# Kernel tuning notes

Measured on AMD Instinct MI355X. Metric: run time of the kernel, lower is better.

Reference implementation:

```python
import jax, jax.numpy as jnp
import numpy as np

H = 1024   # hidden_size == embedding_dim (forced by the 2*hidden concat/view)
A = 256    # attention_hidden_size
V = 50257  # vocab_size
L = 2      # num_layers
T = 512    # decoder length
S = 512    # encoder length


def setup_inputs() -> dict:
    key = jax.random.key(0)
    ks = jax.random.split(key, 24)
    f = lambda i, shape: (0.02 * jax.random.normal(ks[i], shape)).astype(jnp.float32)
    return {
        "decoder_input": jax.random.randint(ks[0], (T,), 0, V),
        "encoder_outputs": jax.random.normal(ks[1], (S, H), dtype=jnp.float32),
        "emb": f(2, (V, H)),
        # attn (context attention over encoder outputs): Linear(2H->A) split into x/ctx parts, v: Linear(A->1)
        "Wa_x": f(3, (A, H)), "Wa_c": f(4, (A, H)), "ba": f(5, (A,)), "va": f(6, (A,)), "vab": f(7, ()),
        # GRU cells (torch GRUCell param layout: [r; z; n] stacked, 3H rows)
        "Wih0": f(8, (3 * H, 2 * H)), "bih0": f(9, (3 * H,)), "Whh0": f(10, (3 * H, H)), "bhh0": f(11, (3 * H,)),
        "Wih1": f(12, (3 * H, H)), "bih1": f(13, (3 * H,)), "Whh1": f(14, (3 * H, H)), "bhh1": f(15, (3 * H,)),
        # per-layer hidden self-attentions (no context)
        "Wh": f(16, (L, A, H)), "bh": f(17, (L, A)), "vh": f(18, (L, A)), "vhb": f(19, (L,)),
        # output head
        "Wf1": f(20, (32, H)), "bf1": f(21, (32,)), "Wf2": f(22, (V, 32)), "bf2": f(23, (V,)),
    }


def _attn(x, Wx, b, v, vb, ctx=None, Wc=None):
    # additive attention: e_t = v . tanh(W_x x_t + W_c c + b); weighted sum over axis 0
    pre = x @ Wx.T + b                      # [T, A]
    if ctx is not None:
        pre = pre + ctx @ Wc.T              # broadcast [A]
    e = jnp.tanh(pre) @ v + vb              # [T]
    return jax.nn.softmax(e) @ x            # [D]


def _gru(x, h, Wih, bih, Whh, bhh):
    gi = Wih @ x + bih
    gh = Whh @ h + bhh
    ir, iz, inn = jnp.split(gi, 3)
    hr, hz, hn = jnp.split(gh, 3)
    r = jax.nn.sigmoid(ir + hr)
    z = jax.nn.sigmoid(iz + hz)
    n = jnp.tanh(inn + r * hn)
    return (1.0 - z) * n + z * h


def reference(decoder_input, encoder_outputs, emb, Wa_x, Wa_c, ba, va, vab,
              Wih0, bih0, Whh0, bhh0, Wih1, bih1, Whh1, bhh1,
              Wh, bh, vh, vhb, Wf1, bf1, Wf2, bf2):
    tok_embs = emb[decoder_input]           # [T, H]

    def step(carry, tok):
        h0, h1 = carry
        a = _attn(encoder_outputs, Wa_x, ba, va, vab, ctx=h0, Wc=Wa_c)  # [H]
        x = jnp.concatenate([a, tok])                                   # [2H]
        nh0 = _gru(x, h0, Wih0, bih0, Whh0, bhh0)
        nh1 = _gru(nh0, h1, Wih1, bih1, Whh1, bhh1)
        # hidden attention i combines new_h_s[i:]
        h0n = _attn(jnp.stack([nh0, nh1]), Wh[0], bh[0], vh[0], vhb[0])
        h1n = _attn(nh1[None, :], Wh[1], bh[1], vh[1], vhb[1])           # softmax over 1 elem == nh1
        fc1 = jax.nn.relu(Wf1 @ h1n + bf1)                               # dropout = eval-mode identity
        out = jax.nn.softmax(Wf2 @ fc1 + bf2)                            # softmax over vocab (dim 0)
        return (h0n, h1n), out

    h0 = jnp.zeros((Whh0.shape[1],), jnp.float32)
    _, outs = jax.lax.scan(step, (h0, h0), tok_embs)
    return outs  # [T, V]
```

## Files before the change

kernel.cpp:

```cpp
#include <hip/hip_runtime.h>
#include <cstdint>
#include <cstddef>

#define T_LEN 512
#define S_LEN 512
#define HID   1024
#define AD    256
#define VOC   50257
#define G3    3072
#define NWG   256
#define NT    512
#define NPART (197*4)

typedef unsigned long long u64;

#define WS_GENC   0
#define WS_GITOK  (WS_GENC + G3*S_LEN)
#define WS_EX     (WS_GITOK + T_LEN*G3)
#define WS_H1     (WS_EX + S_LEN*AD)
#define WS_FC1    (WS_H1 + T_LEN*HID)
#define WS_ROWP   (WS_FC1 + T_LEN*32)
#define WS_INV    (WS_ROWP + T_LEN*NPART)
#define WS_TAGF   (((WS_INV + T_LEN) + 3) & ~3)

#define SP 2
#define TG_NH0 0
#define TG_NH1 (TG_NH0 + 2*1024*SP)
#define TG_W   (TG_NH1 + 2*1024*SP)
#define TG_U0  (TG_W   + 2*512*SP)
#define TG_U1  (TG_U0  + 2*256*SP)
#define TG_E0  (TG_U1  + 2*256*SP)
#define TG_E1  (TG_E0  + 2*256*SP)
#define TG_TOT (TG_E1  + 2*256*SP)

__device__ inline float wred64(float v) {
  v += __shfl_xor(v, 32, 64); v += __shfl_xor(v, 16, 64); v += __shfl_xor(v, 8, 64);
  v += __shfl_xor(v, 4, 64);  v += __shfl_xor(v, 2, 64);  v += __shfl_xor(v, 1, 64);
  return v;
}
__device__ inline float fast_sigmoid(float x) { return 1.f / (1.f + __expf(-x)); }
__device__ inline float fast_tanh(float x) {
  float e = __expf(2.f * x);
  return 1.f - 2.f / (e + 1.f);
}

__device__ inline u64 ald(const u64* p) {
  return __hip_atomic_load(p, __ATOMIC_RELAXED, __HIP_MEMORY_SCOPE_AGENT);
}
__device__ inline void stq(u64* p, float v, unsigned tag) {
  __hip_atomic_store(p, ((u64)tag << 32) | (u64)__float_as_uint(v),
                     __ATOMIC_RELAXED, __HIP_MEMORY_SCOPE_AGENT);
}
__device__ inline float poll1(const u64* p, unsigned tag) {
  u64 x = ald(p);
  while ((unsigned)(x >> 32) != tag) { __builtin_amdgcn_s_sleep(1); x = ald(p); }
  return __uint_as_float((unsigned)x);
}
__device__ inline void poll2(const u64* p0, const u64* p1, unsigned tag, float& r0, float& r1) {
  u64 x0 = ald(p0), x1 = ald(p1);
  while (((unsigned)(x0 >> 32) != tag) | ((unsigned)(x1 >> 32) != tag)) {
    __builtin_amdgcn_s_sleep(1); x0 = ald(p0); x1 = ald(p1);
  }
  r0 = __uint_as_float((unsigned)x0); r1 = __uint_as_float((unsigned)x1);
}
__device__ inline void poll4(const u64* p0, const u64* p1, const u64* p2, const u64* p3,
                             unsigned tag, float& r0, float& r1, float& r2, float& r3) {
  u64 x0 = ald(p0), x1 = ald(p1), x2 = ald(p2), x3 = ald(p3);
  while (((unsigned)(x0 >> 32) != tag) | ((unsigned)(x1 >> 32) != tag) |
         ((unsigned)(x2 >> 32) != tag) | ((unsigned)(x3 >> 32) != tag)) {
    __builtin_amdgcn_s_sleep(1);
    x0 = ald(p0); x1 = ald(p1); x2 = ald(p2); x3 = ald(p3);
  }
  r0 = __uint_as_float((unsigned)x0); r1 = __uint_as_float((unsigned)x1);
  r2 = __uint_as_float((unsigned)x2); r3 = __uint_as_float((unsigned)x3);
}

__device__ inline float qdot4(const float4& a0, const float4& a1, const float4& a2, const float4& a3,
                              const float4& x0, const float4& x1, const float4& x2, const float4& x3) {
  float a = 0.f;
  a = fmaf(a0.x, x0.x, a); a = fmaf(a0.y, x0.y, a); a = fmaf(a0.z, x0.z, a); a = fmaf(a0.w, x0.w, a);
  a = fmaf(a1.x, x1.x, a); a = fmaf(a1.y, x1.y, a); a = fmaf(a1.z, x1.z, a); a = fmaf(a1.w, x1.w, a);
  a = fmaf(a2.x, x2.x, a); a = fmaf(a2.y, x2.y, a); a = fmaf(a2.z, x2.z, a); a = fmaf(a2.w, x2.w, a);
  a = fmaf(a3.x, x3.x, a); a = fmaf(a3.y, x3.y, a); a = fmaf(a3.z, x3.z, a); a = fmaf(a3.w, x3.w, a);
  return a;
}
__device__ inline float qdot2(const float4& a0, const float4& a1,
                              const float4& x0, const float4& x1) {
  float a = 0.f;
  a = fmaf(a0.x, x0.x, a); a = fmaf(a0.y, x0.y, a); a = fmaf(a0.z, x0.z, a); a = fmaf(a0.w, x0.w, a);
  a = fmaf(a1.x, x1.x, a); a = fmaf(a1.y, x1.y, a); a = fmaf(a1.z, x1.z, a); a = fmaf(a1.w, x1.w, a);
  return a;
}

__global__ void k_init(float* ws) {
  u64* TG = (u64*)(ws + WS_TAGF);
  const int i = blockIdx.x * 256 + threadIdx.x;
  if (i < TG_TOT) TG[i] = 0ull;
}

__global__ __launch_bounds__(256) void k_gemm(
    const float* __restrict__ A, int lda, const int* __restrict__ gidx,
    const float* __restrict__ B, int ldb, int kofs,
    const float* __restrict__ bias, float* __restrict__ C, int ldc,
    int M, int N, int act)
{
  __shared__ float As[64][33];
  __shared__ float Bs[64][33];
  const int bm = blockIdx.y * 64, bn = blockIdx.x * 64;
// ... 34 lines not shown
      acc[2][0]=fmaf(a2,b0,acc[2][0]); acc[2][1]=fmaf(a2,b1,acc[2][1]); acc[2][2]=fmaf(a2,b2,acc[2][2]); acc[2][3]=fmaf(a2,b3,acc[2][3]);
      acc[3][0]=fmaf(a3,b0,acc[3][0]); acc[3][1]=fmaf(a3,b1,acc[3][1]); acc[3][2]=fmaf(a3,b2,acc[3][2]); acc[3][3]=fmaf(a3,b3,acc[3][3]);
    }
    __syncthreads();
  }
  #pragma unroll
  for (int i = 0; i < 4; ++i)
    #pragma unroll
    for (int j = 0; j < 4; ++j) {
      const int m = bm + ty*4 + i, n = bn + tx*4 + j;
      if (m < M && n < N) {
        float v = acc[i][j] + (bias ? bias[n] : 0.f);
        if (act == 1) v = fmaxf(v, 0.f);
        C[(size_t)m * ldc + n] = v;
      }
    }
}

__global__ __launch_bounds__(NT) void k_recur(
    float* __restrict__ ws,
    const float* __restrict__ Whh0, const float* __restrict__ bhh0,
    const float* __restrict__ Wih1, const float* __restrict__ bih1,
    const float* __restrict__ Whh1, const float* __restrict__ bhh1,
    const float* __restrict__ Wh,   const float* __restrict__ bh,
    const float* __restrict__ vh,   const float* __restrict__ vhb,
    const float* __restrict__ va,   const float* __restrict__ vab,
    const float* __restrict__ Wac)
{
  const float* Genc  = ws + WS_GENC;
  const float* gitok = ws + WS_GITOK;
  const float* Ex    = ws + WS_EX;
  float* H1 = ws + WS_H1;
  u64* TG   = (u64*)(ws + WS_TAGF);
  u64* tNH0 = TG + TG_NH0;
  u64* tNH1 = TG + TG_NH1;
  u64* tW   = TG + TG_W;
  u64* tU0  = TG + TG_U0;
  u64* tU1  = TG + TG_U1;
  u64* tE0  = TG + TG_E0;
  u64* tE1  = TG + TG_E1;

  const int wg = blockIdx.x, tid = threadIdx.x;
  const int lane = tid & 63, wv = tid >> 6;

  __shared__ float xv[HID];
  __shared__ float wl[S_LEN];
  __shared__ float cb[AD];
  __shared__ float sgh0[12], gh1l[12], sb0[12], sbh1[12], sacc[12];
  __shared__ float sred[8];

  float4 wreg[28];
  if (wv < 6) {
    #pragma unroll
    for (int r = 0; r < 2; ++r) {
      const int lr = 2 * wv + r;
      const int g = (lr >> 2) * HID + wg * 4 + (lr & 3);
      const float4* p0 = (const float4*)(Whh0 + (size_t)g * HID);
      const float4* p1 = (const float4*)(Wih1 + (size_t)g * HID);
      const float4* p2 = (const float4*)(Whh1 + (size_t)g * HID);
      const float4* pg = (const float4*)(Genc + (size_t)g * S_LEN);
      #pragma unroll
      for (int p = 0; p < 4; ++p) {
        wreg[r*4+p]      = p0[p*64 + lane];
        wreg[8 + r*4+p]  = p1[p*64 + lane];
        wreg[16 + r*4+p] = p2[p*64 + lane];
      }
      #pragma unroll
      for (int p = 0; p < 2; ++p) wreg[24 + r*2+p] = pg[p*64 + lane];
    }
  } else {
    const float* Wrow = (wv == 6) ? (Wh + (size_t)wg * HID) : (Wac + (size_t)wg * HID);
    const float4* p0 = (const float4*)Wrow;
    #pragma unroll
    for (int p = 0; p < 4; ++p) wreg[p] = p0[p*64 + lane];
    const int s = 2 * wg + (wv - 6);
    wreg[4] = ((const float4*)(Ex + (size_t)s * AD))[lane];
    wreg[5] = ((const float4*)va)[lane];
  }

  float i1r = 0.f, i1z = 0.f, i1n = 0.f;
  if (tid < 4) {
    const int j = wg * 4 + tid;
    i1r = bih1[j]; i1z = bih1[HID + j]; i1n = bih1[2 * HID + j];
  }
  if (tid < 12) {
    const int g = (tid >> 2) * HID + wg * 4 + (tid & 3);
    sb0[tid] = bhh0[g];
    const float bb = bhh1[g];
    sbh1[tid] = bb;
    gh1l[tid] = bb;
  }
  const float vhW = vh[wg], bhW = bh[wg];
  const float vabv = vab[0], vhb0 = vhb[0];
  __syncthreads();

  const float4* XV4 = (const float4*)xv;
  const float4* WL4 = (const float4*)wl;
  const float4* CB4 = (const float4*)cb;

  #pragma unroll 1
  for (int t = 0; t < T_LEN; ++t) {
    const int c = t & 1, pc = c ^ 1;
    const unsigned tg = (unsigned)(t + 1);
    const unsigned tp = (unsigned)t;

    {
      float a0, a1, b0, b1;
      poll4(tNH0 + (size_t)(pc*1024 + tid)*SP, tNH0 + (size_t)(pc*1024 + 512 + tid)*SP,
            tNH1 + (size_t)(pc*1024 + tid)*SP, tNH1 + (size_t)(pc*1024 + 512 + tid)*SP,
            tp, a0, a1, b0, b1);
      float ep, uu0 = 0.f, uu1 = 0.f;
      if (tid < 256) {
        ep = poll1(tE0 + (size_t)(pc*256 + tid)*SP, tp);
        poll2(tU0 + (size_t)(pc*256 + tid)*SP, tU1 + (size_t)(pc*256 + tid)*SP, tp, uu0, uu1);
      } else {
        ep = poll1(tE1 + (size_t)(pc*256 + tid - 256)*SP, tp);
      }
      ep = wred64(ep);
      if (lane == 0) sred[wv] = ep;
      __syncthreads();
      const float e0s = sred[0] + sred[1] + sred[2] + sred[3] + vhb0;
      const float e1s = sred[4] + sred[5] + sred[6] + sred[7] + vhb0;
      const float ea = __expf(e0s), eb = __expf(e1s);
      const float rs = 1.f / (ea + eb);
      const float al0 = ea * rs, al1 = eb * rs;
      xv[tid]       = al0 * a0 + al1 * b0;
      xv[tid + 512] = al0 * a1 + al1 * b1;
      if (tid < 256) cb[tid] = al0 * uu0 + al1 * uu1;
      __syncthreads();
    }
    float h0j = 0.f;
    if (tid < 4) h0j = xv[wg * 4 + tid];
    if (wv < 6) {
      const float4 x0 = XV4[lane], x1 = XV4[64+lane], x2 = XV4[128+lane], x3 = XV4[192+lane];
      float accA = qdot4(wreg[0], wreg[1], wreg[2], wreg[3], x0, x1, x2, x3);
      float accB = qdot4(wreg[4], wreg[5], wreg[6], wreg[7], x0, x1, x2, x3);
      accA = wred64(accA); accB = wred64(accB);
      if (lane == 0) {
        sgh0[2*wv]     = accA + sb0[2*wv];
        sgh0[2*wv + 1] = accB + sb0[2*wv + 1];
      }
    } else {
      const float4 e4 = wreg[4], v4 = wreg[5], c4 = CB4[lane];
      float acc = v4.x * fast_tanh(e4.x + c4.x) + v4.y * fast_tanh(e4.y + c4.y)
                + v4.z * fast_tanh(e4.z + c4.z) + v4.w * fast_tanh(e4.w + c4.w);
      acc = wred64(acc);
      if (lane == 0)
        stq(tW + (size_t)(c*512 + 2*wg + (wv - 6))*SP, __expf(acc + vabv), tg);
    }

    {
      float g0 = 0.f, g1 = 0.f, g2 = 0.f;
      if (tid < 4) {
        const float* gp = gitok + (size_t)t * G3 + wg * 4 + tid;
        g0 = gp[0]; g1 = gp[HID]; g2 = gp[2 * HID];
      }
      const float wval = poll1(tW + (size_t)(c*512 + tid)*SP, tg);
      wl[tid] = wval;
      __syncthreads();
      float inv = 0.f;
      if (wv == 0) {
        float s = 0.f;
        #pragma unroll
        for (int k = 0; k < 8; ++k) s += wl[lane + 64*k];
        s = wred64(s);
        inv = 1.f / s;
      }
      if (wv < 6) {
        const float4 w0 = WL4[lane], w1 = WL4[64 + lane];
        float accA = qdot2(wreg[24], wreg[25], w0, w1);
        float accB = qdot2(wreg[26], wreg[27], w0, w1);
        accA = wred64(accA); accB = wred64(accB);
        if (lane == 0) { sacc[2*wv] = accA; sacc[2*wv + 1] = accB; }
      }
      __syncthreads();
      if (tid < 4) {
        const float d0 = sacc[tid]     * inv + g0;
        const float d1 = sacc[4 + tid] * inv + g1;
        const float d2 = sacc[8 + tid] * inv + g2;
        const float rg = fast_sigmoid(d0 + sgh0[tid]);
        const float zg = fast_sigmoid(d1 + sgh0[4 + tid]);
        const float ng = fast_tanh(d2 + rg * sgh0[8 + tid]);
        stq(tNH0 + (size_t)(c*1024 + wg*4 + tid)*SP, (1.f - zg) * ng + zg * h0j, tg);
      }
    }

    {
      float oldn = 0.f;
      if (tid < 4) oldn = poll1(tNH1 + (size_t)(pc*1024 + wg*4 + tid)*SP, tp);
      float x0, x1;
      poll2(tNH0 + (size_t)(c*1024 + tid)*SP, tNH0 + (size_t)(c*1024 + 512 + tid)*SP, tg, x0, x1);
      xv[tid] = x0; xv[tid + 512] = x1;
      __syncthreads();
      const float4 y0 = XV4[lane], y1 = XV4[64+lane], y2 = XV4[128+lane], y3 = XV4[192+lane];
      if (wv < 6) {
        float accA = qdot4(wreg[8],  wreg[9],  wreg[10], wreg[11], y0, y1, y2, y3);
        float accB = qdot4(wreg[12], wreg[13], wreg[14], wreg[15], y0, y1, y2, y3);
        accA = wred64(accA); accB = wred64(accB);
        if (lane == 0) { sacc[2*wv] = accA; sacc[2*wv + 1] = accB; }
      } else {
        float acc = qdot4(wreg[0], wreg[1], wreg[2], wreg[3], y0, y1, y2, y3);
        acc = wred64(acc);
        if (lane == 0) {
          if (wv == 6) stq(tE0 + (size_t)(c*256 + wg)*SP, vhW * fast_tanh(acc + bhW), tg);
          else         stq(tU0 + (size_t)(c*256 + wg)*SP, acc, tg);
        }
      }
      __syncthreads();
      if (tid < 4) {
        const float gr = sacc[tid]     + i1r;
        const float gz = sacc[4 + tid] + i1z;
        const float gn = sacc[8 + tid] + i1n;
        const float rg = fast_sigmoid(gr + gh1l[tid]);
        const float zg = fast_sigmoid(gz + gh1l[4 + tid]);
        const float ng = fast_tanh(gn + rg * gh1l[8 + tid]);
        const float nv = (1.f - zg) * ng + zg * oldn;
        stq(tNH1 + (size_t)(c*1024 + wg*4 + tid)*SP, nv, tg);
        H1[(size_t)t * HID + wg * 4 + tid] = nv;
      }
    }

    {
      float x0, x1;
      poll2(tNH1 + (size_t)(c*1024 + tid)*SP, tNH1 + (size_t)(c*1024 + 512 + tid)*SP, tg, x0, x1);
      xv[tid] = x0; xv[tid + 512] = x1;
      __syncthreads();
      const float4 y0 = XV4[lane], y1 = XV4[64+lane], y2 = XV4[128+lane], y3 = XV4[192+lane];
      if (wv < 6) {
        float accA = qdot4(wreg[16], wreg[17], wreg[18], wreg[19], y0, y1, y2, y3);
        float accB = qdot4(wreg[20], wreg[21], wreg[22], wreg[23], y0, y1, y2, y3);
        accA = wred64(accA); accB = wred64(accB);
        if (lane == 0) {
          gh1l[2*wv]     = accA + sbh1[2*wv];
          gh1l[2*wv + 1] = accB + sbh1[2*wv + 1];
        }
      } else {
        float acc = qdot4(wreg[0], wreg[1], wreg[2], wreg[3], y0, y1, y2, y3);
        acc = wred64(acc);
        if (lane == 0) {
          if (wv == 6) stq(tE1 + (size_t)(c*256 + wg)*SP, vhW * fast_tanh(acc + bhW), tg);
          else         stq(tU1 + (size_t)(c*256 + wg)*SP, acc, tg);
        }
      }
    }
  }
}

__global__ __launch_bounds__(256) void k_head(
    const float* __restrict__ FC1, const float* __restrict__ Wf2,
    const float* __restrict__ bf2, float* __restrict__ out, float* __restrict__ rowp)
{
  __shared__ float fcb[256 * 32];
  const int v = blockIdx.x * 256 + threadIdx.x;
  const bool ok = v < VOC;
  float wf[32];
  float bb = 0.f;
  if (ok) {
    const float4* W4 = (const float4*)(Wf2 + (size_t)v * 32);
    #pragma unroll
    for (int q = 0; q < 8; ++q) ((float4*)wf)[q] = W4[q];
    bb = bf2[v];
  }
  const int wv = threadIdx.x >> 6;
  #pragma unroll 1
  for (int half = 0; half < 2; ++half) {
    __syncthreads();
    for (int i = threadIdx.x; i < 256 * 32 / 4; i += 256)
      ((float4*)fcb)[i] = ((const float4*)(FC1 + half * 256 * 32))[i];
    __syncthreads();
    #pragma unroll 1
    for (int tt = 0; tt < 256; ++tt) {
      const int t = half * 256 + tt;
      const float4* f4 = (const float4*)(fcb + tt * 32);
      float acc = bb;
      #pragma unroll
// ... 36 lines not shown
  }
}

extern "C" void kernel_launch(void* const* d_in, const int* in_sizes, int n_in,
                              void* d_out, int out_size, void* d_ws, size_t ws_size,
                              hipStream_t stream) {
  const int*   dec  = (const int*)  d_in[0];
  const float* enc  = (const float*)d_in[1];
  const float* emb  = (const float*)d_in[2];
  const float* Wax  = (const float*)d_in[3];
  const float* Wac  = (const float*)d_in[4];
  const float* ba   = (const float*)d_in[5];
  const float* va   = (const float*)d_in[6];
  const float* vab  = (const float*)d_in[7];
  const float* Wih0 = (const float*)d_in[8];
  const float* bih0 = (const float*)d_in[9];
  const float* Whh0 = (const float*)d_in[10];
  const float* bhh0 = (const float*)d_in[11];
  const float* Wih1 = (const float*)d_in[12];
  const float* bih1 = (const float*)d_in[13];
  const float* Whh1 = (const float*)d_in[14];
  const float* bhh1 = (const float*)d_in[15];
  const float* Wh   = (const float*)d_in[16];
  const float* bh   = (const float*)d_in[17];
  const float* vh   = (const float*)d_in[18];
  const float* vhb  = (const float*)d_in[19];
  const float* Wf1  = (const float*)d_in[20];
  const float* bf1  = (const float*)d_in[21];
  const float* Wf2  = (const float*)d_in[22];
  const float* bf2  = (const float*)d_in[23];
  float* out = (float*)d_out;
  float* ws  = (float*)d_ws;

  k_init<<<56, 256, 0, stream>>>(ws);

  k_gemm<<<dim3(8, 48), 256, 0, stream>>>(Wih0, 2048, nullptr, enc, 1024, 0,
                                          nullptr, ws + WS_GENC, 512, G3, S_LEN, 0);
  k_gemm<<<dim3(48, 8), 256, 0, stream>>>(emb, 1024, dec, Wih0, 2048, 1024,
                                          bih0, ws + WS_GITOK, G3, T_LEN, G3, 0);
  k_gemm<<<dim3(4, 8), 256, 0, stream>>>(enc, 1024, nullptr, Wax, 1024, 0,
                                         ba, ws + WS_EX, AD, S_LEN, AD, 0);

  k_recur<<<NWG, NT, 0, stream>>>(ws, Whh0, bhh0, Wih1, bih1, Whh1, bhh1,
                                  Wh, bh, vh, vhb, va, vab, Wac);

  k_gemm<<<dim3(1, 8), 256, 0, stream>>>(ws + WS_H1, 1024, nullptr, Wf1, 1024, 0,
                                         bf1, ws + WS_FC1, 32, T_LEN, 32, 1);

  k_head<<<197, 256, 0, stream>>>(ws + WS_FC1, Wf2, bf2, out, ws + WS_ROWP);
  k_rowsum<<<512, 256, 0, stream>>>(ws + WS_ROWP, ws + WS_INV);
  k_scale<<<dim3(25, 512), 256, 0, stream>>>(out, ws + WS_INV);
}
```

Baseline: 5.575 ms.

## Restructure GRU recurrence so each wave owns one hidden unit and caches states locally

The persistent recurrent kernel is reorganised so that waves 0-3 each own one hidden index j and hold all three gate rows (r, z, n) of Whh0, Wih1, Whh1 and Genc in registers. Gate activations are now computed in-wave, which removes the shared-memory scratch arrays and the extra __syncthreads round trips that previously gathered partial dot products into a few threads. Each block keeps nh0 and nh1 in two local shared buffers, so the start-of-step polling of all 2048 previous hidden values goes away, along with the separate poll for the old h1 value. Tag slots are packed densely without the stride-2 padding, and the pollers reload only slots that are still pending, with a longer sleep. The cost is higher register pressure from 42 float4 registers per thread, a different wave split for the attention work, and potential contention from unpadded tag slots.

```diff
diff --git a/kernel.cpp b/kernel.cpp
--- a/kernel.cpp
+++ b/kernel.cpp
@@ -23,15 +23,14 @@
 #define WS_INV    (WS_ROWP + T_LEN*NPART)
 #define WS_TAGF   (((WS_INV + T_LEN) + 3) & ~3)
 
-#define SP 2
 #define TG_NH0 0
-#define TG_NH1 (TG_NH0 + 2*1024*SP)
-#define TG_W   (TG_NH1 + 2*1024*SP)
-#define TG_U0  (TG_W   + 2*512*SP)
-#define TG_U1  (TG_U0  + 2*256*SP)
-#define TG_E0  (TG_U1  + 2*256*SP)
-#define TG_E1  (TG_E0  + 2*256*SP)
-#define TG_TOT (TG_E1  + 2*256*SP)
+#define TG_NH1 (TG_NH0 + 2*1024)
+#define TG_W   (TG_NH1 + 2*1024)
+#define TG_U0  (TG_W   + 2*512)
+#define TG_U1  (TG_U0  + 2*256)
+#define TG_E0  (TG_U1  + 2*256)
+#define TG_E1  (TG_E0  + 2*256)
+#define TG_TOT (TG_E1  + 2*256)
 
 __device__ inline float wred64(float v) {
   v += __shfl_xor(v, 32, 64); v += __shfl_xor(v, 16, 64); v += __shfl_xor(v, 8, 64);
@@ -51,28 +50,38 @@
   __hip_atomic_store(p, ((u64)tag << 32) | (u64)__float_as_uint(v),
                      __ATOMIC_RELAXED, __HIP_MEMORY_SCOPE_AGENT);
 }
-__device__ inline float poll1(const u64* p, unsigned tag) {
+__device__ inline float pollw(const u64* p, unsigned tag) {
   u64 x = ald(p);
-  while ((unsigned)(x >> 32) != tag) { __builtin_amdgcn_s_sleep(1); x = ald(p); }
+  while ((unsigned)(x >> 32) != tag) { __builtin_amdgcn_s_sleep(2); x = ald(p); }
   return __uint_as_float((unsigned)x);
 }
-__device__ inline void poll2(const u64* p0, const u64* p1, unsigned tag, float& r0, float& r1) {
+__device__ inline void poll2e(const u64* p0, const u64* p1, unsigned tag, float& r0, float& r1) {
   u64 x0 = ald(p0), x1 = ald(p1);
-  while (((unsigned)(x0 >> 32) != tag) | ((unsigned)(x1 >> 32) != tag)) {
-    __builtin_amdgcn_s_sleep(1); x0 = ald(p0); x1 = ald(p1);
+  while (true) {
+    const bool d0 = ((unsigned)(x0 >> 32) == tag);
+    const bool d1 = ((unsigned)(x1 >> 32) == tag);
+    if (d0 & d1) break;
+    __builtin_amdgcn_s_sleep(2);
+    if (!d0) x0 = ald(p0);
+    if (!d1) x1 = ald(p1);
   }
   r0 = __uint_as_float((unsigned)x0); r1 = __uint_as_float((unsigned)x1);
 }
-__device__ inline void poll4(const u64* p0, const u64* p1, const u64* p2, const u64* p3,
-                             unsigned tag, float& r0, float& r1, float& r2, float& r3) {
-  u64 x0 = ald(p0), x1 = ald(p1), x2 = ald(p2), x3 = ald(p3);
-  while (((unsigned)(x0 >> 32) != tag) | ((unsigned)(x1 >> 32) != tag) |
-         ((unsigned)(x2 >> 32) != tag) | ((unsigned)(x3 >> 32) != tag)) {
-    __builtin_amdgcn_s_sleep(1);
-    x0 = ald(p0); x1 = ald(p1); x2 = ald(p2); x3 = ald(p3);
+__device__ inline void poll3e(const u64* p0, const u64* p1, const u64* p2, unsigned tag,
+                              float& r0, float& r1, float& r2) {
+  u64 x0 = ald(p0), x1 = ald(p1), x2 = ald(p2);
+  while (true) {
+    const bool d0 = ((unsigned)(x0 >> 32) == tag);
+    const bool d1 = ((unsigned)(x1 >> 32) == tag);
+    const bool d2 = ((unsigned)(x2 >> 32) == tag);
+    if (d0 & d1 & d2) break;
+    __builtin_amdgcn_s_sleep(2);
+    if (!d0) x0 = ald(p0);
+    if (!d1) x1 = ald(p1);
+    if (!d2) x2 = ald(p2);
   }
   r0 = __uint_as_float((unsigned)x0); r1 = __uint_as_float((unsigned)x1);
-  r2 = __uint_as_float((unsigned)x2); r3 = __uint_as_float((unsigned)x3);
+  r2 = __uint_as_float((unsigned)x2);
 }
 
 __device__ inline float qdot4(const float4& a0, const float4& a1, const float4& a2, const float4& a3,
@@ -184,61 +193,61 @@
 
   const int wg = blockIdx.x, tid = threadIdx.x;
   const int lane = tid & 63, wv = tid >> 6;
-
-  __shared__ float xv[HID];
+  const int j = wg * 4 + wv;
+
+  __shared__ float xva[HID];
+  __shared__ float xvb[HID];
   __shared__ float wl[S_LEN];
   __shared__ float cb[AD];
-  __shared__ float sgh0[12], gh1l[12], sb0[12], sbh1[12], sacc[12];
   __shared__ float sred[8];
 
-  float4 wreg[28];
-  if (wv < 6) {
+  float4 wreg[42];
+  if (wv < 4) {
     #pragma unroll
-    for (int r = 0; r < 2; ++r) {
-      const int lr = 2 * wv + r;
-      const int g = (lr >> 2) * HID + wg * 4 + (lr & 3);
+    for (int r3 = 0; r3 < 3; ++r3) {
+      const int g = r3 * HID + j;
       const float4* p0 = (const float4*)(Whh0 + (size_t)g * HID);
       const float4* p1 = (const float4*)(Wih1 + (size_t)g * HID);
       const float4* p2 = (const float4*)(Whh1 + (size_t)g * HID);
       const float4* pg = (const float4*)(Genc + (size_t)g * S_LEN);
       #pragma unroll
       for (int p = 0; p < 4; ++p) {
-        wreg[r*4+p]      = p0[p*64 + lane];
-        wreg[8 + r*4+p]  = p1[p*64 + lane];
-        wreg[16 + r*4+p] = p2[p*64 + lane];
-      }
-      #pragma unroll
-      for (int p = 0; p < 2; ++p) wreg[24 + r*2+p] = pg[p*64 + lane];
-    }
+        wreg[r3*4 + p]      = p0[p*64 + lane];
+        wreg[12 + r3*4 + p] = p1[p*64 + lane];
+        wreg[24 + r3*4 + p] = p2[p*64 + lane];
+      }
+      wreg[36 + r3*2]     = pg[lane];
+      wreg[36 + r3*2 + 1] = pg[64 + lane];
+    }
+  } else if (wv < 6) {
+    const int s = 2 * wg + (wv - 4);
+    wreg[0] = ((const float4*)(Ex + (size_t)s * AD))[lane];
+    wreg[1] = ((const float4*)va)[lane];
   } else {
     const float* Wrow = (wv == 6) ? (Wh + (size_t)wg * HID) : (Wac + (size_t)wg * HID);
-    const float4* p0 = (const float4*)Wrow;
     #pragma unroll
-    for (int p = 0; p < 4; ++p) wreg[p] = p0[p*64 + lane];
-    const int s = 2 * wg + (wv - 6);
-    wreg[4] = ((const float4*)(Ex + (size_t)s * AD))[lane];
-    wreg[5] = ((const float4*)va)[lane];
-  }
-
-  float i1r = 0.f, i1z = 0.f, i1n = 0.f;
-  if (tid < 4) {
-    const int j = wg * 4 + tid;
-    i1r = bih1[j]; i1z = bih1[HID + j]; i1n = bih1[2 * HID + j];
-  }
-  if (tid < 12) {
-    const int g = (tid >> 2) * HID + wg * 4 + (tid & 3);
-    sb0[tid] = bhh0[g];
-    const float bb = bhh1[g];
-    sbh1[tid] = bb;
-    gh1l[tid] = bb;
+    for (int p = 0; p < 4; ++p) wreg[p] = ((const float4*)Wrow)[p*64 + lane];
+  }
+
+  float b0r=0,b0z=0,b0n=0, c1r=0,c1z=0,c1n=0, bh1r=0,bh1z=0,bh1n=0;
+  float gh1r=0, gh1z=0, gh1n=0, oldn=0.f;
+  if (wv < 4) {
+    b0r = bhh0[j];  b0z = bhh0[HID+j];  b0n = bhh0[2*HID+j];
+    c1r = bih1[j];  c1z = bih1[HID+j];  c1n = bih1[2*HID+j];
+    bh1r = bhh1[j]; bh1z = bhh1[HID+j]; bh1n = bhh1[2*HID+j];
+    gh1r = bh1r; gh1z = bh1z; gh1n = bh1n;
   }
   const float vhW = vh[wg], bhW = bh[wg];
   const float vabv = vab[0], vhb0 = vhb[0];
+
+  xva[tid] = 0.f; xva[tid+512] = 0.f;
+  xvb[tid] = 0.f; xvb[tid+512] = 0.f;
   __syncthreads();
 
-  const float4* XV4 = (const float4*)xv;
+  float gh0r = 0.f, gh0z = 0.f, gh0n = 0.f;
+  const float4* XA4 = (const float4*)xva;
+  const float4* XB4 = (const float4*)xvb;
   const float4* WL4 = (const float4*)wl;
-  const float4* CB4 = (const float4*)cb;
 
   #pragma unroll 1
   for (int t = 0; t < T_LEN; ++t) {
@@ -247,141 +256,109 @@
     const unsigned tp = (unsigned)t;
 
     {
-      float a0, a1, b0, b1;
-      poll4(tNH0 + (size_t)(pc*1024 + tid)*SP, tNH0 + (size_t)(pc*1024 + 512 + tid)*SP,
-            tNH1 + (size_t)(pc*1024 + tid)*SP, tNH1 + (size_t)(pc*1024 + 512 + tid)*SP,
-            tp, a0, a1, b0, b1);
       float ep, uu0 = 0.f, uu1 = 0.f;
       if (tid < 256) {
-        ep = poll1(tE0 + (size_t)(pc*256 + tid)*SP, tp);
-        poll2(tU0 + (size_t)(pc*256 + tid)*SP, tU1 + (size_t)(pc*256 + tid)*SP, tp, uu0, uu1);
+        poll3e(tE0 + pc*256 + tid, tU0 + pc*256 + tid, tU1 + pc*256 + tid, tp, ep, uu0, uu1);
       } else {
-        ep = poll1(tE1 + (size_t)(pc*256 + tid - 256)*SP, tp);
-      }
-      ep = wred64(ep);
-      if (lane == 0) sred[wv] = ep;
+        ep = pollw(tE1 + pc*256 + (tid - 256), tp);
+      }
+      float eps = wred64(ep);
+      if (lane == 0) sred[wv] = eps;
       __syncthreads();
-      const float e0s = sred[0] + sred[1] + sred[2] + sred[3] + vhb0;
-      const float e1s = sred[4] + sred[5] + sred[6] + sred[7] + vhb0;
+      const float e0s = sred[0]+sred[1]+sred[2]+sred[3] + vhb0;
+      const float e1s = sred[4]+sred[5]+sred[6]+sred[7] + vhb0;
       const float ea = __expf(e0s), eb = __expf(e1s);
       const float rs = 1.f / (ea + eb);
       const float al0 = ea * rs, al1 = eb * rs;
-      xv[tid]       = al0 * a0 + al1 * b0;
-      xv[tid + 512] = al0 * a1 + al1 * b1;
+      const float h0 = al0 * xva[tid]       + al1 * xvb[tid];
+      const float h1 = al0 * xva[tid + 512] + al1 * xvb[tid + 512];
+      xva[tid] = h0; xva[tid + 512] = h1;
       if (tid < 256) cb[tid] = al0 * uu0 + al1 * uu1;
       __syncthreads();
-    }
-    float h0j = 0.f;
-    if (tid < 4) h0j = xv[wg * 4 + tid];
-    if (wv < 6) {
-      const float4 x0 = XV4[lane], x1 = XV4[64+lane], x2 = XV4[128+lane], x3 = XV4[192+lane];
-      float accA = qdot4(wreg[0], wreg[1], wreg[2], wreg[3], x0, x1, x2, x3);
-      float accB = qdot4(wreg[4], wreg[5], wreg[6], wreg[7], x0, x1, x2, x3);
-      accA = wred64(accA); accB = wred64(accB);
-      if (lane == 0) {
-        sgh0[2*wv]     = accA + sb0[2*wv];
-        sgh0[2*wv + 1] = accB + sb0[2*wv + 1];
-      }
-    } else {
-      const float4 e4 = wreg[4], v4 = wreg[5], c4 = CB4[lane];
-      float acc = v4.x * fast_tanh(e4.x + c4.x) + v4.y * fast_tanh(e4.y + c4.y)
-                + v4.z * fast_tanh(e4.z + c4.z) + v4.w * fast_tanh(e4.w + c4.w);
-      acc = wred64(acc);
-      if (lane == 0)
-        stq(tW + (size_t)(c*512 + 2*wg + (wv - 6))*SP, __expf(acc + vabv), tg);
+      if (wv < 4) {
+        const float4 x0 = XA4[lane], x1 = XA4[64+lane], x2 = XA4[128+lane], x3 = XA4[192+lane];
+        gh0r = wred64(qdot4(wreg[0], wreg[1], wreg[2],  wreg[3],  x0,x1,x2,x3)) + b0r;
+        gh0z = wred64(qdot4(wreg[4], wreg[5], wreg[6],  wreg[7],  x0,x1,x2,x3)) + b0z;
+        gh0n = wred64(qdot4(wreg[8], wreg[9], wreg[10], wreg[11], x0,x1,x2,x3)) + b0n;
+      } else if (wv < 6) {
+        const float4 e4 = wreg[0], v4 = wreg[1];
+        const float4 c4 = ((const float4*)cb)[lane];
+        float acc = v4.x * fast_tanh(e4.x + c4.x) + v4.y * fast_tanh(e4.y + c4.y)
+                  + v4.z * fast_tanh(e4.z + c4.z) + v4.w * fast_tanh(e4.w + c4.w);
+        acc = wred64(acc);
+        if (lane == 0) stq(tW + c*512 + 2*wg + (wv - 4), __expf(acc + vabv), tg);
+      }
     }
 
     {
       float g0 = 0.f, g1 = 0.f, g2 = 0.f;
-      if (tid < 4) {
-        const float* gp = gitok + (size_t)t * G3 + wg * 4 + tid;
-        g0 = gp[0]; g1 = gp[HID]; g2 = gp[2 * HID];
-      }
-      const float wval = poll1(tW + (size_t)(c*512 + tid)*SP, tg);
-      wl[tid] = wval;
+      if (wv < 4) {
+        const float* gp = gitok + (size_t)t * G3 + j;
+        g0 = gp[0]; g1 = gp[HID]; g2 = gp[2*HID];
+      }
+      const float wvv = pollw(tW + c*512 + tid, tg);
+      wl[tid] = wvv;
       __syncthreads();
-      float inv = 0.f;
-      if (wv == 0) {
-        float s = 0.f;
-        #pragma unroll
-        for (int k = 0; k < 8; ++k) s += wl[lane + 64*k];
-        s = wred64(s);
-        inv = 1.f / s;
-      }
-      if (wv < 6) {
+      if (wv < 4) {
         const float4 w0 = WL4[lane], w1 = WL4[64 + lane];
-        float accA = qdot2(wreg[24], wreg[25], w0, w1);
-        float accB = qdot2(wreg[26], wreg[27], w0, w1);
-        accA = wred64(accA); accB = wred64(accB);
-        if (lane == 0) { sacc[2*wv] = accA; sacc[2*wv + 1] = accB; }
-      }
+        float sw = w0.x+w0.y+w0.z+w0.w + w1.x+w1.y+w1.z+w1.w;
+        sw = wred64(sw);
+        const float inv = 1.f / sw;
+        const float d0 = wred64(qdot2(wreg[36], wreg[37], w0, w1));
+        const float d1 = wred64(qdot2(wreg[38], wreg[39], w0, w1));
+        const float d2 = wred64(qdot2(wreg[40], wreg[41], w0, w1));
+        const float rg = fast_sigmoid(d0*inv + g0 + gh0r);
+        const float zg = fast_sigmoid(d1*inv + g1 + gh0z);
+        const float ng = fast_tanh(d2*inv + g2 + rg * gh0n);
+        const float h0j = xva[j];
+        const float nv = (1.f - zg) * ng + zg * h0j;
+        if (lane == 0) stq(tNH0 + c*1024 + j, nv, tg);
+      }
+    }
+
+    {
+      float x0, x1;
+      poll2e(tNH0 + c*1024 + tid, tNH0 + c*1024 + 512 + tid, tg, x0, x1);
+      xva[tid] = x0; xva[tid + 512] = x1;
       __syncthreads();
-      if (tid < 4) {
-        const float d0 = sacc[tid]     * inv + g0;
-        const float d1 = sacc[4 + tid] * inv + g1;
-        const float d2 = sacc[8 + tid] * inv + g2;
-        const float rg = fast_sigmoid(d0 + sgh0[tid]);
-        const float zg = fast_sigmoid(d1 + sgh0[4 + tid]);
-        const float ng = fast_tanh(d2 + rg * sgh0[8 + tid]);
-        stq(tNH0 + (size_t)(c*1024 + wg*4 + tid)*SP, (1.f - zg) * ng + zg * h0j, tg);
-      }
-    }
-
-    {
-      float oldn = 0.f;
-      if (tid < 4) oldn = poll1(tNH1 + (size_t)(pc*1024 + wg*4 + tid)*SP, tp);
+      const float4 y0 = XA4[lane], y1 = XA4[64+lane], y2 = XA4[128+lane], y3 = XA4[192+lane];
+      if (wv < 4) {
+        const float a0 = wred64(qdot4(wreg[12], wreg[13], wreg[14], wreg[15], y0,y1,y2,y3));
+        const float a1 = wred64(qdot4(wreg[16], wreg[17], wreg[18], wreg[19], y0,y1,y2,y3));
+        const float a2 = wred64(qdot4(wreg[20], wreg[21], wreg[22], wreg[23], y0,y1,y2,y3));
+        const float rg = fast_sigmoid(a0 + c1r + gh1r);
+        const float zg = fast_sigmoid(a1 + c1z + gh1z);
+        const float ng = fast_tanh(a2 + c1n + rg * gh1n);
+        const float nv = (1.f - zg) * ng + zg * oldn;
+        oldn = nv;
+        if (lane == 0) {
+          stq(tNH1 + c*1024 + j, nv, tg);
+          H1[(size_t)t * HID + j] = nv;
+        }
+      } else if (wv >= 6) {
+        float acc = wred64(qdot4(wreg[0], wreg[1], wreg[2], wreg[3], y0,y1,y2,y3));
+        if (lane == 0) {
+          if (wv == 6) stq(tE0 + c*256 + wg, vhW * fast_tanh(acc + bhW), tg);
+          else         stq(tU0 + c*256 + wg, acc, tg);
+        }
+      }
+    }
+
+    {
       float x0, x1;
-      poll2(tNH0 + (size_t)(c*1024 + tid)*SP, tNH0 + (size_t)(c*1024 + 512 + tid)*SP, tg, x0, x1);
-      xv[tid] = x0; xv[tid + 512] = x1;
+      poll2e(tNH1 + c*1024 + tid, tNH1 + c*1024 + 512 + tid, tg, x0, x1);
+      xvb[tid] = x0; xvb[tid + 512] = x1;
       __syncthreads();
-      const float4 y0 = XV4[lane], y1 = XV4[64+lane], y2 = XV4[128+lane], y3 = XV4[192+lane];
-      if (wv < 6) {
-        float accA = qdot4(wreg[8],  wreg[9],  wreg[10], wreg[11], y0, y1, y2, y3);
-        float accB = qdot4(wreg[12], wreg[13], wreg[14], wreg[15], y0, y1, y2, y3);
-        accA = wred64(accA); accB = wred64(accB);
-        if (lane == 0) { sacc[2*wv] = accA; sacc[2*wv + 1] = accB; }
-      } else {
-        float acc = qdot4(wreg[0], wreg[1], wreg[2], wreg[3], y0, y1, y2, y3);
-        acc = wred64(acc);
+      const float4 y0 = XB4[lane], y1 = XB4[64+lane], y2 = XB4[128+lane], y3 = XB4[192+lane];
+      if (wv < 4) {
+        gh1r = wred64(qdot4(wreg[24], wreg[25], wreg[26], wreg[27], y0,y1,y2,y3)) + bh1r;
+        gh1z = wred64(qdot4(wreg[28], wreg[29], wreg[30], wreg[31], y0,y1,y2,y3)) + bh1z;
+        gh1n = wred64(qdot4(wreg[32], wreg[33], wreg[34], wreg[35], y0,y1,y2,y3)) + bh1n;
+      } else if (wv >= 6) {
+        float acc = wred64(qdot4(wreg[0], wreg[1], wreg[2], wreg[3], y0,y1,y2,y3));
         if (lane == 0) {
-          if (wv == 6) stq(tE0 + (size_t)(c*256 + wg)*SP, vhW * fast_tanh(acc + bhW), tg);
-          else         stq(tU0 + (size_t)(c*256 + wg)*SP, acc, tg);
-        }
-      }
-      __syncthreads();
-      if (tid < 4) {
-        const float gr = sacc[tid]     + i1r;
-        const float gz = sacc[4 + tid] + i1z;
-        const float gn = sacc[8 + tid] + i1n;
-        const float rg = fast_sigmoid(gr + gh1l[tid]);
-        const float zg = fast_sigmoid(gz + gh1l[4 + tid]);
-        const float ng = fast_tanh(gn + rg * gh1l[8 + tid]);
-        const float nv = (1.f - zg) * ng + zg * oldn;
-        stq(tNH1 + (size_t)(c*1024 + wg*4 + tid)*SP, nv, tg);
-        H1[(size_t)t * HID + wg * 4 + tid] = nv;
-      }
-    }
-
-    {
-      float x0, x1;
-      poll2(tNH1 + (size_t)(c*1024 + tid)*SP, tNH1 + (size_t)(c*1024 + 512 + tid)*SP, tg, x0, x1);
-      xv[tid] = x0; xv[tid + 512] = x1;
-      __syncthreads();
-      const float4 y0 = XV4[lane], y1 = XV4[64+lane], y2 = XV4[128+lane], y3 = XV4[192+lane];
-      if (wv < 6) {
-        float accA = qdot4(wreg[16], wreg[17], wreg[18], wreg[19], y0, y1, y2, y3);
-        float accB = qdot4(wreg[20], wreg[21], wreg[22], wreg[23], y0, y1, y2, y3);
-        accA = wred64(accA); accB = wred64(accB);
-        if (lane == 0) {
-          gh1l[2*wv]     = accA + sbh1[2*wv];
-          gh1l[2*wv + 1] = accB + sbh1[2*wv + 1];
-        }
-      } else {
-        float acc = qdot4(wreg[0], wreg[1], wreg[2], wreg[3], y0, y1, y2, y3);
-        acc = wred64(acc);
-        if (lane == 0) {
-          if (wv == 6) stq(tE1 + (size_t)(c*256 + wg)*SP, vhW * fast_tanh(acc + bhW), tg);
-          else         stq(tU1 + (size_t)(c*256 + wg)*SP, acc, tg);
+          if (wv == 6) stq(tE1 + c*256 + wg, vhW * fast_tanh(acc + bhW), tg);
+          else         stq(tU1 + c*256 + wg, acc, tg);
         }
       }
     }
@@ -485,7 +462,7 @@
   float* out = (float*)d_out;
   float* ws  = (float*)d_ws;
 
-  k_init<<<56, 256, 0, stream>>>(ws);
+  k_init<<<28, 256, 0, stream>>>(ws);
 
   k_gemm<<<dim3(8, 48), 256, 0, stream>>>(Wih0, 2048, nullptr, enc, 1024, 0,
                                           nullptr, ws + WS_GENC, 512, G3, S_LEN, 0);
```

Result: slower. 8.255 ms (+48.1%).

## Pack per-workgroup tagged flags into 64-byte lines and keep hidden states in shared memory

Applied to the files above, without the earlier changes.

Replaces the strided per-element tag slots with one 64-byte record per workgroup per parity, so each polling lane reads four contiguous tagged values instead of scattered ones. The E0/E1/U0/U1 scalars are merged into a single record, and only four waves poll while the rest wait at a barrier. Previous hidden states are kept in two shared buffers (xva/xvb), so the extra polls for the old h0/h1 values are no longer needed. The aim is to cut cross-workgroup flag traffic and polling latency on the serial recurrence, at the cost of added __syncthreads barriers.

```diff
diff --git a/kernel.cpp b/kernel.cpp
--- a/kernel.cpp
+++ b/kernel.cpp
@@ -21,17 +21,13 @@
 #define WS_FC1    (WS_H1 + T_LEN*HID)
 #define WS_ROWP   (WS_FC1 + T_LEN*32)
 #define WS_INV    (WS_ROWP + T_LEN*NPART)
-#define WS_TAGF   (((WS_INV + T_LEN) + 3) & ~3)
-
-#define SP 2
-#define TG_NH0 0
-#define TG_NH1 (TG_NH0 + 2*1024*SP)
-#define TG_W   (TG_NH1 + 2*1024*SP)
-#define TG_U0  (TG_W   + 2*512*SP)
-#define TG_U1  (TG_U0  + 2*256*SP)
-#define TG_E0  (TG_U1  + 2*256*SP)
-#define TG_E1  (TG_E0  + 2*256*SP)
-#define TG_TOT (TG_E1  + 2*256*SP)
+#define WS_TAGF   (((WS_INV + T_LEN) + 15) & ~15)
+
+#define TG_EU  0
+#define TG_W   (TG_EU  + 2*NWG*8)
+#define TG_NH0 (TG_W   + 2*NWG*8)
+#define TG_NH1 (TG_NH0 + 2*NWG*8)
+#define TG_TOT (TG_NH1 + 2*NWG*8)
 
 __device__ inline float wred64(float v) {
   v += __shfl_xor(v, 32, 64); v += __shfl_xor(v, 16, 64); v += __shfl_xor(v, 8, 64);
@@ -51,29 +47,8 @@
   __hip_atomic_store(p, ((u64)tag << 32) | (u64)__float_as_uint(v),
                      __ATOMIC_RELAXED, __HIP_MEMORY_SCOPE_AGENT);
 }
-__device__ inline float poll1(const u64* p, unsigned tag) {
-  u64 x = ald(p);
-  while ((unsigned)(x >> 32) != tag) { __builtin_amdgcn_s_sleep(1); x = ald(p); }
-  return __uint_as_float((unsigned)x);
-}
-__device__ inline void poll2(const u64* p0, const u64* p1, unsigned tag, float& r0, float& r1) {
-  u64 x0 = ald(p0), x1 = ald(p1);
-  while (((unsigned)(x0 >> 32) != tag) | ((unsigned)(x1 >> 32) != tag)) {
-    __builtin_amdgcn_s_sleep(1); x0 = ald(p0); x1 = ald(p1);
-  }
-  r0 = __uint_as_float((unsigned)x0); r1 = __uint_as_float((unsigned)x1);
-}
-__device__ inline void poll4(const u64* p0, const u64* p1, const u64* p2, const u64* p3,
-                             unsigned tag, float& r0, float& r1, float& r2, float& r3) {
-  u64 x0 = ald(p0), x1 = ald(p1), x2 = ald(p2), x3 = ald(p3);
-  while (((unsigned)(x0 >> 32) != tag) | ((unsigned)(x1 >> 32) != tag) |
-         ((unsigned)(x2 >> 32) != tag) | ((unsigned)(x3 >> 32) != tag)) {
-    __builtin_amdgcn_s_sleep(1);
-    x0 = ald(p0); x1 = ald(p1); x2 = ald(p2); x3 = ald(p3);
-  }
-  r0 = __uint_as_float((unsigned)x0); r1 = __uint_as_float((unsigned)x1);
-  r2 = __uint_as_float((unsigned)x2); r3 = __uint_as_float((unsigned)x3);
-}
+#define LO_F(x) __uint_as_float((unsigned)(x))
+#define TAGOK(x, t) (((unsigned)((x) >> 32)) == (t))
 
 __device__ inline float qdot4(const float4& a0, const float4& a1, const float4& a2, const float4& a3,
                               const float4& x0, const float4& x1, const float4& x2, const float4& x3) {
@@ -174,22 +149,21 @@
   const float* Ex    = ws + WS_EX;
   float* H1 = ws + WS_H1;
   u64* TG   = (u64*)(ws + WS_TAGF);
+  u64* tEU  = TG + TG_EU;
+  u64* tW   = TG + TG_W;
   u64* tNH0 = TG + TG_NH0;
   u64* tNH1 = TG + TG_NH1;
-  u64* tW   = TG + TG_W;
-  u64* tU0  = TG + TG_U0;
-  u64* tU1  = TG + TG_U1;
-  u64* tE0  = TG + TG_E0;
-  u64* tE1  = TG + TG_E1;
 
   const int wg = blockIdx.x, tid = threadIdx.x;
   const int lane = tid & 63, wv = tid >> 6;
 
-  __shared__ float xv[HID];
+  __shared__ float xva[HID];
+  __shared__ float xvb[HID];
   __shared__ float wl[S_LEN];
   __shared__ float cb[AD];
-  __shared__ float sgh0[12], gh1l[12], sb0[12], sbh1[12], sacc[12];
-  __shared__ float sred[8];
+  __shared__ float e0l[NWG], e1l[NWG], u0l[NWG], u1l[NWG];
+  __shared__ float sgh0[12], sacc[12], gh1l[12], sb0[12], sbh1[12], sbi1[12];
+  __shared__ float sred[4];
 
   float4 wreg[28];
   if (wv < 6) {
@@ -220,23 +194,23 @@
     wreg[5] = ((const float4*)va)[lane];
   }
 
-  float i1r = 0.f, i1z = 0.f, i1n = 0.f;
-  if (tid < 4) {
-    const int j = wg * 4 + tid;
-    i1r = bih1[j]; i1z = bih1[HID + j]; i1n = bih1[2 * HID + j];
-  }
   if (tid < 12) {
     const int g = (tid >> 2) * HID + wg * 4 + (tid & 3);
-    sb0[tid] = bhh0[g];
+    sb0[tid]  = bhh0[g];
+    sbi1[tid] = bih1[g];
     const float bb = bhh1[g];
     sbh1[tid] = bb;
     gh1l[tid] = bb;
   }
   const float vhW = vh[wg], bhW = bh[wg];
   const float vabv = vab[0], vhb0 = vhb[0];
+
+  xva[tid] = 0.f; xva[tid + 512] = 0.f;
+  xvb[tid] = 0.f; xvb[tid + 512] = 0.f;
   __syncthreads();
 
-  const float4* XV4 = (const float4*)xv;
+  const float4* XA4 = (const float4*)xva;
+  const float4* XB4 = (const float4*)xvb;
   const float4* WL4 = (const float4*)wl;
   const float4* CB4 = (const float4*)cb;
 
@@ -247,48 +221,55 @@
     const unsigned tp = (unsigned)t;
 
     {
-      float a0, a1, b0, b1;
-      poll4(tNH0 + (size_t)(pc*1024 + tid)*SP, tNH0 + (size_t)(pc*1024 + 512 + tid)*SP,
-            tNH1 + (size_t)(pc*1024 + tid)*SP, tNH1 + (size_t)(pc*1024 + 512 + tid)*SP,
-            tp, a0, a1, b0, b1);
-      float ep, uu0 = 0.f, uu1 = 0.f;
-      if (tid < 256) {
-        ep = poll1(tE0 + (size_t)(pc*256 + tid)*SP, tp);
-        poll2(tU0 + (size_t)(pc*256 + tid)*SP, tU1 + (size_t)(pc*256 + tid)*SP, tp, uu0, uu1);
-      } else {
-        ep = poll1(tE1 + (size_t)(pc*256 + tid - 256)*SP, tp);
-      }
-      ep = wred64(ep);
-      if (lane == 0) sred[wv] = ep;
-      __syncthreads();
-      const float e0s = sred[0] + sred[1] + sred[2] + sred[3] + vhb0;
-      const float e1s = sred[4] + sred[5] + sred[6] + sred[7] + vhb0;
-      const float ea = __expf(e0s), eb = __expf(e1s);
+      if (wv < 4) {
+        const int q = (wv << 6) | lane;
+        const u64* L = tEU + ((size_t)pc * NWG + q) * 8;
+        u64 x0, x1, x2, x3;
+        for (;;) {
+          x0 = ald(L); x1 = ald(L + 1); x2 = ald(L + 2); x3 = ald(L + 3);
+          if (TAGOK(x0, tp) & TAGOK(x1, tp) & TAGOK(x2, tp) & TAGOK(x3, tp)) break;
+          __builtin_amdgcn_s_sleep(1);
+        }
+        e0l[q] = LO_F(x0); e1l[q] = LO_F(x1); u0l[q] = LO_F(x2); u1l[q] = LO_F(x3);
+      }
+      __syncthreads();
+      if (wv == 0) {
+        float a = e0l[lane] + e0l[64 + lane] + e0l[128 + lane] + e0l[192 + lane];
+        a = wred64(a);
+        if (lane == 0) sred[0] = a;
+      } else if (wv == 1) {
+        float a = e1l[lane] + e1l[64 + lane] + e1l[128 + lane] + e1l[192 + lane];
+        a = wred64(a);
+        if (lane == 0) sred[1] = a;
+      }
+      __syncthreads();
+      const float ea = __expf(sred[0] + vhb0), eb = __expf(sred[1] + vhb0);
       const float rs = 1.f / (ea + eb);
       const float al0 = ea * rs, al1 = eb * rs;
-      xv[tid]       = al0 * a0 + al1 * b0;
-      xv[tid + 512] = al0 * a1 + al1 * b1;
-      if (tid < 256) cb[tid] = al0 * uu0 + al1 * uu1;
-      __syncthreads();
-    }
-    float h0j = 0.f;
-    if (tid < 4) h0j = xv[wg * 4 + tid];
-    if (wv < 6) {
-      const float4 x0 = XV4[lane], x1 = XV4[64+lane], x2 = XV4[128+lane], x3 = XV4[192+lane];
-      float accA = qdot4(wreg[0], wreg[1], wreg[2], wreg[3], x0, x1, x2, x3);
-      float accB = qdot4(wreg[4], wreg[5], wreg[6], wreg[7], x0, x1, x2, x3);
-      accA = wred64(accA); accB = wred64(accB);
-      if (lane == 0) {
-        sgh0[2*wv]     = accA + sb0[2*wv];
-        sgh0[2*wv + 1] = accB + sb0[2*wv + 1];
-      }
-    } else {
-      const float4 e4 = wreg[4], v4 = wreg[5], c4 = CB4[lane];
-      float acc = v4.x * fast_tanh(e4.x + c4.x) + v4.y * fast_tanh(e4.y + c4.y)
-                + v4.z * fast_tanh(e4.z + c4.z) + v4.w * fast_tanh(e4.w + c4.w);
-      acc = wred64(acc);
-      if (lane == 0)
-        stq(tW + (size_t)(c*512 + 2*wg + (wv - 6))*SP, __expf(acc + vabv), tg);
+      {
+        const float h0 = al0 * xva[tid]       + al1 * xvb[tid];
+        const float h1 = al0 * xva[tid + 512] + al1 * xvb[tid + 512];
+        xva[tid] = h0; xva[tid + 512] = h1;
+      }
+      if (tid < AD) cb[tid] = al0 * u0l[tid] + al1 * u1l[tid];
+      __syncthreads();
+      if (wv < 6) {
+        const float4 x0 = XA4[lane], x1 = XA4[64+lane], x2 = XA4[128+lane], x3 = XA4[192+lane];
+        float accA = qdot4(wreg[0], wreg[1], wreg[2], wreg[3], x0, x1, x2, x3);
+        float accB = qdot4(wreg[4], wreg[5], wreg[6], wreg[7], x0, x1, x2, x3);
+        accA = wred64(accA); accB = wred64(accB);
+        if (lane == 0) {
+          sgh0[2*wv]     = accA + sb0[2*wv];
+          sgh0[2*wv + 1] = accB + sb0[2*wv + 1];
+        }
+      } else {
+        const float4 e4 = wreg[4], v4 = wreg[5], c4 = CB4[lane];
+        float acc = v4.x * fast_tanh(e4.x + c4.x) + v4.y * fast_tanh(e4.y + c4.y)
+                  + v4.z * fast_tanh(e4.z + c4.z) + v4.w * fast_tanh(e4.w + c4.w);
+        acc = wred64(acc);
+        if (lane == 0)
+          stq(tW + ((size_t)c * NWG + wg) * 8 + (wv - 6), __expf(acc + vabv), tg);
+      }
     }
 
     {
@@ -297,16 +278,24 @@
         const float* gp = gitok + (size_t)t * G3 + wg * 4 + tid;
         g0 = gp[0]; g1 = gp[HID]; g2 = gp[2 * HID];
       }
-      const float wval = poll1(tW + (size_t)(c*512 + tid)*SP, tg);
-      wl[tid] = wval;
-      __syncthreads();
-      float inv = 0.f;
-      if (wv == 0) {
+      if (wv < 4) {
+        const int q = (wv << 6) | lane;
+        const u64* L = tW + ((size_t)c * NWG + q) * 8;
+        u64 x0, x1;
+        for (;;) {
+          x0 = ald(L); x1 = ald(L + 1);
+          if (TAGOK(x0, tg) & TAGOK(x1, tg)) break;
+          __builtin_amdgcn_s_sleep(1);
+        }
+        wl[2*q] = LO_F(x0); wl[2*q + 1] = LO_F(x1);
+      }
+      __syncthreads();
+      if (wv == 1) {
         float s = 0.f;
         #pragma unroll
-        for (int k = 0; k < 8; ++k) s += wl[lane + 64*k];
+        for (int k = 0; k < 8; ++k) s += wl[lane + 64 * k];
         s = wred64(s);
-        inv = 1.f / s;
+        if (lane == 0) sred[2] = s;
       }
       if (wv < 6) {
         const float4 w0 = WL4[lane], w1 = WL4[64 + lane];
@@ -317,57 +306,78 @@
       }
       __syncthreads();
       if (tid < 4) {
+        const float inv = 1.f / sred[2];
         const float d0 = sacc[tid]     * inv + g0;
         const float d1 = sacc[4 + tid] * inv + g1;
         const float d2 = sacc[8 + tid] * inv + g2;
         const float rg = fast_sigmoid(d0 + sgh0[tid]);
         const float zg = fast_sigmoid(d1 + sgh0[4 + tid]);
         const float ng = fast_tanh(d2 + rg * sgh0[8 + tid]);
-        stq(tNH0 + (size_t)(c*1024 + wg*4 + tid)*SP, (1.f - zg) * ng + zg * h0j, tg);
-      }
-    }
-
+        const float nv = (1.f - zg) * ng + zg * xva[wg * 4 + tid];
+        stq(tNH0 + ((size_t)c * NWG + wg) * 8 + tid, nv, tg);
+      }
+    }
+
+    __syncthreads();
     {
-      float oldn = 0.f;
-      if (tid < 4) oldn = poll1(tNH1 + (size_t)(pc*1024 + wg*4 + tid)*SP, tp);
-      float x0, x1;
-      poll2(tNH0 + (size_t)(c*1024 + tid)*SP, tNH0 + (size_t)(c*1024 + 512 + tid)*SP, tg, x0, x1);
-      xv[tid] = x0; xv[tid + 512] = x1;
-      __syncthreads();
-      const float4 y0 = XV4[lane], y1 = XV4[64+lane], y2 = XV4[128+lane], y3 = XV4[192+lane];
+      if (wv < 4) {
+        const int q = (wv << 6) | lane;
+        const u64* L = tNH0 + ((size_t)c * NWG + q) * 8;
+        u64 x0, x1, x2, x3;
+        for (;;) {
+          x0 = ald(L); x1 = ald(L + 1); x2 = ald(L + 2); x3 = ald(L + 3);
+          if (TAGOK(x0, tg) & TAGOK(x1, tg) & TAGOK(x2, tg) & TAGOK(x3, tg)) break;
+          __builtin_amdgcn_s_sleep(1);
+        }
+        float4 v; v.x = LO_F(x0); v.y = LO_F(x1); v.z = LO_F(x2); v.w = LO_F(x3);
+        ((float4*)xva)[q] = v;
+      }
+      __syncthreads();
+      const float4 y0 = XA4[lane], y1 = XA4[64+lane], y2 = XA4[128+lane], y3 = XA4[192+lane];
       if (wv < 6) {
         float accA = qdot4(wreg[8],  wreg[9],  wreg[10], wreg[11], y0, y1, y2, y3);
         float accB = qdot4(wreg[12], wreg[13], wreg[14], wreg[15], y0, y1, y2, y3);
         accA = wred64(accA); accB = wred64(accB);
         if (lane == 0) { sacc[2*wv] = accA; sacc[2*wv + 1] = accB; }
+      } else if (wv == 6) {
+        float acc = wred64(qdot4(wreg[0], wreg[1], wreg[2], wreg[3], y0, y1, y2, y3));
+        if (lane == 0)
+          stq(tEU + ((size_t)c * NWG + wg) * 8 + 0, vhW * fast_tanh(acc + bhW), tg);
       } else {
-        float acc = qdot4(wreg[0], wreg[1], wreg[2], wreg[3], y0, y1, y2, y3);
-        acc = wred64(acc);
-        if (lane == 0) {
-          if (wv == 6) stq(tE0 + (size_t)(c*256 + wg)*SP, vhW * fast_tanh(acc + bhW), tg);
-          else         stq(tU0 + (size_t)(c*256 + wg)*SP, acc, tg);
-        }
+        float acc = wred64(qdot4(wreg[0], wreg[1], wreg[2], wreg[3], y0, y1, y2, y3));
+        if (lane == 0)
+          stq(tEU + ((size_t)c * NWG + wg) * 8 + 2, acc, tg);
       }
       __syncthreads();
       if (tid < 4) {
-        const float gr = sacc[tid]     + i1r;
-        const float gz = sacc[4 + tid] + i1z;
-        const float gn = sacc[8 + tid] + i1n;
+        const float gr = sacc[tid]     + sbi1[tid];
+        const float gz = sacc[4 + tid] + sbi1[4 + tid];
+        const float gn = sacc[8 + tid] + sbi1[8 + tid];
         const float rg = fast_sigmoid(gr + gh1l[tid]);
         const float zg = fast_sigmoid(gz + gh1l[4 + tid]);
         const float ng = fast_tanh(gn + rg * gh1l[8 + tid]);
-        const float nv = (1.f - zg) * ng + zg * oldn;
-        stq(tNH1 + (size_t)(c*1024 + wg*4 + tid)*SP, nv, tg);
+        const float nv = (1.f - zg) * ng + zg * xvb[wg * 4 + tid];
+        stq(tNH1 + ((size_t)c * NWG + wg) * 8 + tid, nv, tg);
         H1[(size_t)t * HID + wg * 4 + tid] = nv;
       }
     }
 
+    __syncthreads();
     {
-      float x0, x1;
-      poll2(tNH1 + (size_t)(c*1024 + tid)*SP, tNH1 + (size_t)(c*1024 + 512 + tid)*SP, tg, x0, x1);
-      xv[tid] = x0; xv[tid + 512] = x1;
-      __syncthreads();
-      const float4 y0 = XV4[lane], y1 = XV4[64+lane], y2 = XV4[128+lane], y3 = XV4[192+lane];
+      if (wv < 4) {
+        const int q = (wv << 6) | lane;
+        const u64* L = tNH1 + ((size_t)c * NWG + q) * 8;
+        u64 x0, x1, x2, x3;
+        for (;;) {
+          x0 = ald(L); x1 = ald(L + 1); x2 = ald(L + 2); x3 = ald(L + 3);
+          if (TAGOK(x0, tg) & TAGOK(x1, tg) & TAGOK(x2, tg) & TAGOK(x3, tg)) break;
+          __builtin_amdgcn_s_sleep(1);
+        }
+        float4 v; v.x = LO_F(x0); v.y = LO_F(x1); v.z = LO_F(x2); v.w = LO_F(x3);
+        ((float4*)xvb)[q] = v;
+      }
+      __syncthreads();
+      const float4 y0 = XB4[lane], y1 = XB4[64+lane], y2 = XB4[128+lane], y3 = XB4[192+lane];
       if (wv < 6) {
         float accA = qdot4(wreg[16], wreg[17], wreg[18], wreg[19], y0, y1, y2, y3);
         float accB = qdot4(wreg[20], wreg[21], wreg[22], wreg[23], y0, y1, y2, y3);
@@ -376,13 +386,14 @@
           gh1l[2*wv]     = accA + sbh1[2*wv];
           gh1l[2*wv + 1] = accB + sbh1[2*wv + 1];
         }
+      } else if (wv == 6) {
+        float acc = wred64(qdot4(wreg[0], wreg[1], wreg[2], wreg[3], y0, y1, y2, y3));
+        if (lane == 0)
+          stq(tEU + ((size_t)c * NWG + wg) * 8 + 1, vhW * fast_tanh(acc + bhW), tg);
       } else {
-        float acc = qdot4(wreg[0], wreg[1], wreg[2], wreg[3], y0, y1, y2, y3);
-        acc = wred64(acc);
-        if (lane == 0) {
-          if (wv == 6) stq(tE1 + (size_t)(c*256 + wg)*SP, vhW * fast_tanh(acc + bhW), tg);
-          else         stq(tU1 + (size_t)(c*256 + wg)*SP, acc, tg);
-        }
+        float acc = wred64(qdot4(wreg[0], wreg[1], wreg[2], wreg[3], y0, y1, y2, y3));
+        if (lane == 0)
+          stq(tEU + ((size_t)c * NWG + wg) * 8 + 3, acc, tg);
       }
     }
   }
@@ -485,7 +496,7 @@
   float* out = (float*)d_out;
   float* ws  = (float*)d_ws;
 
-  k_init<<<56, 256, 0, stream>>>(ws);
+  k_init<<<64, 256, 0, stream>>>(ws);
 
   k_gemm<<<dim3(8, 48), 256, 0, stream>>>(Wih0, 2048, nullptr, enc, 1024, 0,
                                           nullptr, ws + WS_GENC, 512, G3, S_LEN, 0);
```

Measured after the change: 7.442 ms. +33.5%, slower.
